# Performance work log

Measured on AMD Instinct MI355X. Metric: run time of the kernel, lower is better.

The kernel has to match this reference:

```python
import jax, jax.numpy as jnp
import numpy as np

NA, NW, H = 20000, 100000, 128
DA, DW = 64, 128
E_CR, E_IN, E_CO = 400000, 600000, 300000


def _seg_softmax(logits, seg, n):
    m = jax.ops.segment_max(logits, seg, num_segments=n)
    e = jnp.exp(logits - m[seg])
    s = jax.ops.segment_sum(e, seg, num_segments=n)
    return e / (s[seg] + 1e-16)


def _gat(x_src, x_dst, edge, W, b, a_s, a_d):
    # PyG GATConv, heads=1, concat=False, shared lin for src/dst, add_self_loops=True
    n_src, n_dst = x_src.shape[0], x_dst.shape[0]
    loops = jnp.arange(min(n_src, n_dst), dtype=edge.dtype)
    src = jnp.concatenate([edge[0], loops])
    dst = jnp.concatenate([edge[1], loops])
    hs = x_src @ W            # [n_src, H]
    hd = x_dst @ W            # [n_dst, H]
    logit = jax.nn.leaky_relu((hs @ a_s)[src] + (hd @ a_d)[dst], 0.2)
    alpha = _seg_softmax(logit, dst, n_dst)          # softmax over in-neighborhoods
    out = jax.ops.segment_sum(alpha[:, None] * hs[src], dst, num_segments=n_dst)
    return out + b


def _mlp2(x, w1, b1, w2, b2):
    return jax.nn.relu(x @ w1 + b1) @ w2 + b2


def setup_inputs() -> dict:
    key = jax.random.key(0)
    ks = iter(jax.random.split(key, 40))

    def p(shape, scale=0.1):
        return jax.random.normal(next(ks), shape, jnp.float32) * scale

    def edges(n_src, n_dst, E):
        s = jax.random.randint(next(ks), (E,), 0, n_src, dtype=jnp.int32)
        d = jax.random.randint(next(ks), (E,), 0, n_dst, dtype=jnp.int32)
        d = jnp.where(s == d, (d + 1) % n_dst, d)  # keep input loop-free (PyG strips them)
        return jnp.stack([s, d])

    e_creates = edges(NA, NW, E_CR)
    inp = {
        'artist_feat': jax.random.normal(next(ks), (NA, DA), jnp.float32),
        'work_feat': jax.random.normal(next(ks), (NW, DW), jnp.float32),
        'a_w1': p((DA, H)), 'a_b1': jnp.zeros(H, jnp.float32),
        'a_w2': p((H, H)), 'a_b2': jnp.zeros(H, jnp.float32),
        'w_w1': p((DW, H)), 'w_b1': jnp.zeros(H, jnp.float32),
        'w_w2': p((H, H)), 'w_b2': jnp.zeros(H, jnp.float32),
        'cr_W': p((H, H)), 'cr_b': jnp.zeros(H, jnp.float32), 'cr_as': p((H,)), 'cr_ad': p((H,)),
        'in_W': p((H, H)), 'in_b': jnp.zeros(H, jnp.float32), 'in_as': p((H,)), 'in_ad': p((H,)),
        'co_W': p((H, H)), 'co_b': jnp.zeros(H, jnp.float32), 'co_as': p((H,)), 'co_ad': p((H,)),
        'p_w1': p((2 * H, 256)), 'p_b1': jnp.zeros(256, jnp.float32),
        'p_w2': p((256, 128)), 'p_b2': jnp.zeros(128, jnp.float32),
        'p_w3': p((128, 1)), 'p_b3': jnp.zeros(1, jnp.float32),
        'e_creates': e_creates,
        'e_created_by': jnp.flip(e_creates, axis=0),  # reverse relation [work, artist]
        'e_infl': edges(NW, NW, E_IN),
        'e_collab': edges(NA, NA, E_CO),
    }
    return inp


def reference(artist_feat, work_feat,
              a_w1, a_b1, a_w2, a_b2,
              w_w1, w_b1, w_w2, w_b2,
              cr_W, cr_b, cr_as, cr_ad,
              in_W, in_b, in_as, in_ad,
              co_W, co_b, co_as, co_ad,
              p_w1, p_b1, p_w2, p_b2, p_w3, p_b3,
              e_creates, e_created_by, e_infl, e_collab):
    ax = _mlp2(artist_feat, a_w1, a_b1, a_w2, a_b2)      # [NA, H]
    wx = _mlp2(work_feat, w_w1, w_b1, w_w2, w_b2)        # [NW, H]
    wx = jax.nn.elu(_gat(ax, wx, e_creates, cr_W, cr_b, cr_as, cr_ad))
    wx = jax.nn.elu(_gat(wx, wx, e_infl, in_W, in_b, in_as, in_ad))
    au = _gat(wx, ax, e_created_by, cr_W, cr_b, cr_as, cr_ad)  # no elu (matches source)
    ac = jax.nn.elu(_gat(au, au, e_collab, co_W, co_b, co_as, co_ad))
    comb = jnp.concatenate([au, ac], axis=1)             # [NA, 2H]
    h = jax.nn.relu(comb @ p_w1 + p_b1)                  # dropout is identity in eval
    h = jax.nn.relu(h @ p_w2 + p_b2)
    return (h @ p_w3 + p_b3).squeeze()
```

## Files before the change

### kernel.cpp

```cpp
#include <hip/hip_runtime.h>
#include <hip/hip_bf16.h>
#include <cstddef>

#define NA 20000
#define NW 100000
#define HH 128
#define DA 64
#define E_CR 400000
#define E_IN 600000
#define E_CO 300000

#define ROW1 0
#define ROW2 (NW)
#define ROW3 (2 * NW)
#define ROW4 (2 * NW + NA)
#define NTOT (2 * NW + 2 * NA)
#define CAPW 40
#define CAPA 88
#define NPREP (10 * 128 + 1)
#define GNB ((NA + 127) / 128)

typedef short v8s __attribute__((ext_vector_type(8)));
typedef float v4f __attribute__((ext_vector_type(4)));

constexpr int PSLOT = 2 * 128 * 264;

__device__ inline short f2bf(float x) {
    union { float f; unsigned u; } c; c.f = x;
    unsigned r = c.u + 0x7fff + ((c.u >> 16) & 1);
    return (short)(r >> 16);
}
__device__ inline float bf2f(short s) {
    union { unsigned u; float f; } c; c.u = ((unsigned)(unsigned short)s) << 16;
    return c.f;
}
__device__ inline float bfu2f(unsigned short s) {
    union { unsigned u; float f; } c; c.u = ((unsigned)s) << 16;
    return c.f;
}

__device__ inline void split8(const float* xv, v8s& h, v8s& l) {
#pragma unroll
    for (int p = 0; p < 4; ++p) {
        float2 xf; xf.x = xv[2 * p]; xf.y = xv[2 * p + 1];
        __hip_bfloat162 hb = __float22bfloat162_rn(xf);
        float2 hf = __bfloat1622float2(hb);
        float2 lf; lf.x = xf.x - hf.x; lf.y = xf.y - hf.y;
        __hip_bfloat162 lb = __float22bfloat162_rn(lf);
        union { __hip_bfloat162 b; short2 s; } uh, ul;
        uh.b = hb; ul.b = lb;
        h[2 * p] = uh.s.x; h[2 * p + 1] = uh.s.y;
        l[2 * p] = ul.s.x; l[2 * p + 1] = ul.s.y;
    }
}

struct AppChunk { const int* e; int E; int* pad; int cap; int* deg; };

__device__ inline void do_append(const AppChunk& ap, int bid) {
    int b0 = bid * 1024 + threadIdx.x;
    int s[4], d[4]; bool ok[4];
#pragma unroll
    for (int u = 0; u < 4; ++u) {
        int i = b0 + u * 256;
        ok[u] = i < ap.E;
        s[u] = 0; d[u] = 0;
        if (ok[u]) { s[u] = ap.e[i]; d[u] = ap.e[ap.E + i]; }
    }
    int p[4];
#pragma unroll
    for (int u = 0; u < 4; ++u) if (ok[u]) p[u] = atomicAdd(&ap.deg[d[u]], 1);
#pragma unroll
    for (int u = 0; u < 4; ++u)
        if (ok[u] && p[u] < ap.cap)
            ap.pad[(size_t)d[u] * ap.cap + p[u]] = s[u];
}

struct PrepDesc { const float* src; int ldw; int K; };
struct PrepArgs {
    PrepDesc d[10]; const float* wvW; const float* wvA; float* vd;
    const float* gX; const float* gB; float* gY; int gM;
};

__global__ __launch_bounds__(256) void k_prep_append(PrepArgs a, short* __restrict__ out,
                                                    AppChunk ap)
{
    __shared__ short Bs2[2 * 128 * 72];
    if (blockIdx.x >= NPREP + GNB) { do_append(ap, blockIdx.x - NPREP - GNB); return; }
    if (blockIdx.x >= NPREP) {
        int bid = blockIdx.x - NPREP;
        const int tid = threadIdx.x;
        const int wave = tid >> 6, lane = tid & 63;
        const int l15 = lane & 15, quad = lane >> 4;
        const int wrow = bid * 128 + wave * 32;
        for (int e = tid; e < 64 * 128; e += 256) {
            int n = e & 127, k = e >> 7;
            float x = a.d[0].src[(size_t)k * 128 + n];
            short h = f2bf(x);
            short l = f2bf(x - bf2f(h));
            Bs2[n * 72 + k] = h;
            Bs2[128 * 72 + n * 72 + k] = l;
        }
        v8s ah[2][2], al[2][2];
#pragma unroll
        for (int rf = 0; rf < 2; ++rf) {
            int r = wrow + rf * 16 + l15; if (r >= a.gM) r = a.gM - 1;
            const float* xp = a.gX + (size_t)r * DA + quad * 8;
#pragma unroll
            for (int kf = 0; kf < 2; ++kf) {
                float xv[8];
                *(float4*)&xv[0] = *(const float4*)(xp + kf * 32);
                *(float4*)&xv[4] = *(const float4*)(xp + kf * 32 + 4);
                split8(xv, ah[rf][kf], al[rf][kf]);
            }
        }
        __syncthreads();
        v4f acc[2][8];
#pragma unroll
        for (int rf = 0; rf < 2; ++rf)
#pragma unroll
            for (int cf = 0; cf < 8; ++cf) acc[rf][cf] = (v4f){0.f, 0.f, 0.f, 0.f};
#pragma unroll
        for (int kf = 0; kf < 2; ++kf) {
#pragma unroll
            for (int cf = 0; cf < 8; ++cf) {
                int coff = (cf * 16 + l15) * 72 + kf * 32 + quad * 8;
                v8s bh = *(const v8s*)&Bs2[coff];
                v8s bl = *(const v8s*)&Bs2[128 * 72 + coff];
#pragma unroll
                for (int rf = 0; rf < 2; ++rf) {
                    acc[rf][cf] = __builtin_amdgcn_mfma_f32_16x16x32_bf16(al[rf][kf], bh, acc[rf][cf], 0, 0, 0);
                    acc[rf][cf] = __builtin_amdgcn_mfma_f32_16x16x32_bf16(ah[rf][kf], bl, acc[rf][cf], 0, 0, 0);
                    acc[rf][cf] = __builtin_amdgcn_mfma_f32_16x16x32_bf16(ah[rf][kf], bh, acc[rf][cf], 0, 0, 0);
                }
            }
        }
        float bv[8];
#pragma unroll
        for (int cf = 0; cf < 8; ++cf) bv[cf] = a.gB[cf * 16 + l15];
#pragma unroll
        for (int rf = 0; rf < 2; ++rf) {
#pragma unroll
            for (int reg = 0; reg < 4; ++reg) {
                int r = wrow + rf * 16 + quad * 4 + reg;
                if (r >= a.gM) continue;
                float* yp = a.gY + (size_t)r * HH;
#pragma unroll
                for (int cf = 0; cf < 8; ++cf) {
                    float o = acc[rf][cf][reg] + bv[cf];
                    yp[cf * 16 + l15] = o > 0.f ? o : 0.f;
                }
            }
        }
        return;
    }
    if (blockIdx.x == NPREP - 1) {
        __shared__ float sa[HH];
        int t = threadIdx.x;
        if (t < HH) sa[t] = a.wvA[t];
        __syncthreads();
        if (t < HH) {
            float s = 0.f;
            for (int jj = 0; jj < HH; ++jj) s += a.wvW[(size_t)t * HH + jj] * sa[jj];
            a.vd[t] = s;
        }
        return;
    }
    int m = blockIdx.x >> 7;
    int e = (blockIdx.x & 127) * 256 + threadIdx.x;
    PrepDesc dd = a.d[m];
    int K = dd.K;
    int KP = (K <= 128) ? K + 8 : K;
    if (e >= K * 128) return;
    int n = e & 127, k = e >> 7;
    float x = dd.src[(size_t)k * dd.ldw + n];
    short h = f2bf(x);
    short l = f2bf(x - bf2f(h));
    short* base = out + (size_t)m * PSLOT;
    base[n * KP + k] = h;
    base[128 * KP + n * KP + k] = l;
}

template<int K, int ACT, int NSS, int ST, int LDSB, int OBF, int DUAL>
__global__ __launch_bounds__(256, 2) void k_mfma(
    const float* __restrict__ X, int ldx,
    const short* __restrict__ Wp,
    const float* __restrict__ bias,
    float* __restrict__ Y, int ldy, int M,
    const float* __restrict__ v1, float* __restrict__ ss1,
    const float* __restrict__ v2, float* __restrict__ ss2,
    const float* __restrict__ sb)
{
    constexpr int KF = K / 32;
    constexpr int KP = LDSB ? K + 8 : K;
    __shared__ short Bs[LDSB ? 2 * 128 * (K + 8) : 8];
    const int tid = threadIdx.x;
    const int wave = tid >> 6, lane = tid & 63;
    const int l15 = lane & 15, quad = lane >> 4;
    int bid = blockIdx.x;
    if (DUAL) {
        int g0 = gridDim.x >> 1;
        if (bid >= g0) { bid -= g0; Wp += PSLOT; bias += 128; Y += 128; }
    }
    const int wrow = bid * 128 + wave * 32;

    if (LDSB) {
        const float4* src = (const float4*)Wp;
        float4* dst = (float4*)Bs;
        constexpr int total = 2 * 128 * KP / 8;
        for (int i = tid; i < total; i += 256) dst[i] = src[i];
    }

    v4f acc[2][8];
#pragma unroll
    for (int rf = 0; rf < 2; ++rf)
#pragma unroll
        for (int cf = 0; cf < 8; ++cf) acc[rf][cf] = (v4f){0.f, 0.f, 0.f, 0.f};

    if (LDSB) {
        v8s ah[2][KF], al[2][KF];
#pragma unroll
        for (int rf = 0; rf < 2; ++rf) {
            int r = wrow + rf * 16 + l15; if (r >= M) r = M - 1;
            const float* xp = X + (size_t)r * ldx + quad * 8;
#pragma unroll
            for (int kf = 0; kf < KF; ++kf) {
                float xv[8];
                *(float4*)&xv[0] = *(const float4*)(xp + kf * 32);
                *(float4*)&xv[4] = *(const float4*)(xp + kf * 32 + 4);
                split8(xv, ah[rf][kf], al[rf][kf]);
            }
        }
        __syncthreads();
#pragma unroll
        for (int kf = 0; kf < KF; ++kf) {
#pragma unroll
            for (int cf = 0; cf < 8; ++cf) {
                const short* bp = &Bs[(cf * 16 + l15) * KP + kf * 32 + quad * 8];
                v8s bh = *(const v8s*)bp;
                v8s bl = *(const v8s*)(bp + 128 * KP);
#pragma unroll
                for (int rf = 0; rf < 2; ++rf) {
                    acc[rf][cf] = __builtin_amdgcn_mfma_f32_16x16x32_bf16(al[rf][kf], bh, acc[rf][cf], 0, 0, 0);
                    acc[rf][cf] = __builtin_amdgcn_mfma_f32_16x16x32_bf16(ah[rf][kf], bl, acc[rf][cf], 0, 0, 0);
                    acc[rf][cf] = __builtin_amdgcn_mfma_f32_16x16x32_bf16(ah[rf][kf], bh, acc[rf][cf], 0, 0, 0);
                }
            }
        }
    } else {
        for (int kf = 0; kf < KF; ++kf) {
            v8s ah[2], al[2];
#pragma unroll
            for (int rf = 0; rf < 2; ++rf) {
                int r = wrow + rf * 16 + l15; if (r >= M) r = M - 1;
                const float* xp = X + (size_t)r * ldx + kf * 32 + quad * 8;
                float xv[8];
                *(float4*)&xv[0] = *(const float4*)xp;
                *(float4*)&xv[4] = *(const float4*)(xp + 4);
                split8(xv, ah[rf], al[rf]);
            }
#pragma unroll
            for (int cf = 0; cf < 8; ++cf) {
                const short* bp = Wp + (size_t)(cf * 16 + l15) * K + kf * 32 + quad * 8;
                v8s bh = *(const v8s*)bp;
                v8s bl = *(const v8s*)(bp + 128 * KP);
#pragma unroll
                for (int rf = 0; rf < 2; ++rf) {
                    acc[rf][cf] = __builtin_amdgcn_mfma_f32_16x16x32_bf16(al[rf], bh, acc[rf][cf], 0, 0, 0);
                    acc[rf][cf] = __builtin_amdgcn_mfma_f32_16x16x32_bf16(ah[rf], bl, acc[rf][cf], 0, 0, 0);
                    acc[rf][cf] = __builtin_amdgcn_mfma_f32_16x16x32_bf16(ah[rf], bh, acc[rf][cf], 0, 0, 0);
                }
            }
        }
    }

    float bv[8], v1c[8], v2c[8];
#pragma unroll
    for (int cf = 0; cf < 8; ++cf) {
        int col = cf * 16 + l15;
        bv[cf] = bias ? bias[col] : 0.f;
        if (NSS >= 1) v1c[cf] = v1[col];
        if (NSS >= 2) v2c[cf] = v2[col];
    }
    float sbv = (NSS >= 1 && sb) ? sb[0] : 0.f;

#pragma unroll
    for (int rf = 0; rf < 2; ++rf) {
#pragma unroll
        for (int reg = 0; reg < 4; ++reg) {
            int r = wrow + rf * 16 + quad * 4 + reg;
            if (r >= M) continue;
            float p1 = 0.f, p2 = 0.f;
#pragma unroll
            for (int cf = 0; cf < 8; ++cf) {
                float o = acc[rf][cf][reg] + bv[cf];
                if (ACT == 1) o = o > 0.f ? o : 0.f;
                if (NSS >= 1) p1 = fmaf(o, v1c[cf], p1);
                if (NSS >= 2) p2 = fmaf(o, v2c[cf], p2);
                if (ST) {
                    if (OBF) ((unsigned short*)Y)[(size_t)r * ldy + cf * 16 + l15] = (unsigned short)f2bf(o);
                    else     Y[(size_t)r * ldy + cf * 16 + l15] = o;
                }
            }
            if (NSS >= 1) {
#pragma unroll
                for (int w = 1; w < 16; w <<= 1) {
                    p1 += __shfl_xor(p1, w, 64);
                    if (NSS >= 2) p2 += __shfl_xor(p2, w, 64);
                }
                if (l15 == 0) {
                    ss1[r] = p1 + sbv;
                    if (NSS >= 2) ss2[r] = p2;
                }
            }
        }
    }
}

struct MfmaCfg {
    const float* X; int ldx;
    const short* Wp;
    const float* bias;
    float* Y; int ldy; int M;
    int act, nss, obf;
    const float* v1; float* ss1;
    const float* v2; float* ss2;
    int nblocks;
};

__global__ __launch_bounds__(256, 2) void k_mfma2(MfmaCfg c0, MfmaCfg c1, AppChunk ap)
{
    constexpr int KF = 4, KP = 136;
    __shared__ short Bs[2 * 128 * KP];
    int bid = blockIdx.x;
    if (bid >= c0.nblocks + c1.nblocks) { do_append(ap, bid - c0.nblocks - c1.nblocks); return; }
    const bool first = bid < c0.nblocks;
    const MfmaCfg& c = first ? c0 : c1;
    if (!first) bid -= c0.nblocks;
    const int tid = threadIdx.x;
    const int wave = tid >> 6, lane = tid & 63;
    const int l15 = lane & 15, quad = lane >> 4;
    const int wrow = bid * 128 + wave * 32;

    {
        const float4* src = (const float4*)c.Wp;
        float4* dst = (float4*)Bs;
        constexpr int total = 2 * 128 * KP / 8;
        for (int i = tid; i < total; i += 256) dst[i] = src[i];
    }

    v4f acc[2][8];
#pragma unroll
    for (int rf = 0; rf < 2; ++rf)
#pragma unroll
        for (int cf = 0; cf < 8; ++cf) acc[rf][cf] = (v4f){0.f, 0.f, 0.f, 0.f};

    v8s ah[2][KF], al[2][KF];
#pragma unroll
    for (int rf = 0; rf < 2; ++rf) {
        int r = wrow + rf * 16 + l15; if (r >= c.M) r = c.M - 1;
        const float* xp = c.X + (size_t)r * c.ldx + quad * 8;
#pragma unroll
        for (int kf = 0; kf < KF; ++kf) {
            float xv[8];
            *(float4*)&xv[0] = *(const float4*)(xp + kf * 32);
            *(float4*)&xv[4] = *(const float4*)(xp + kf * 32 + 4);
            split8(xv, ah[rf][kf], al[rf][kf]);
        }
    }
    __syncthreads();
#pragma unroll
    for (int kf = 0; kf < KF; ++kf) {
#pragma unroll
        for (int cf = 0; cf < 8; ++cf) {
            const short* bp = &Bs[(cf * 16 + l15) * KP + kf * 32 + quad * 8];
            v8s bh = *(const v8s*)bp;
            v8s bl = *(const v8s*)(bp + 128 * KP);
#pragma unroll
            for (int rf = 0; rf < 2; ++rf) {
                acc[rf][cf] = __builtin_amdgcn_mfma_f32_16x16x32_bf16(al[rf][kf], bh, acc[rf][cf], 0, 0, 0);
                acc[rf][cf] = __builtin_amdgcn_mfma_f32_16x16x32_bf16(ah[rf][kf], bl, acc[rf][cf], 0, 0, 0);
                acc[rf][cf] = __builtin_amdgcn_mfma_f32_16x16x32_bf16(ah[rf][kf], bh, acc[rf][cf], 0, 0, 0);
            }
        }
    }

    float bv[8], v1c[8], v2c[8];
#pragma unroll
    for (int cf = 0; cf < 8; ++cf) {
        int col = cf * 16 + l15;
        bv[cf] = c.bias ? c.bias[col] : 0.f;
        v1c[cf] = (c.nss >= 1) ? c.v1[col] : 0.f;
        v2c[cf] = (c.nss >= 2) ? c.v2[col] : 0.f;
    }

#pragma unroll
    for (int rf = 0; rf < 2; ++rf) {
#pragma unroll
        for (int reg = 0; reg < 4; ++reg) {
            int r = wrow + rf * 16 + quad * 4 + reg;
            if (r >= c.M) continue;
            float p1 = 0.f, p2 = 0.f;
#pragma unroll
            for (int cf = 0; cf < 8; ++cf) {
                float o = acc[rf][cf][reg] + bv[cf];
                if (c.act) o = o > 0.f ? o : 0.f;
                p1 = fmaf(o, v1c[cf], p1);
                p2 = fmaf(o, v2c[cf], p2);
                if (c.obf) ((unsigned short*)c.Y)[(size_t)r * c.ldy + cf * 16 + l15] = (unsigned short)f2bf(o);
                else       c.Y[(size_t)r * c.ldy + cf * 16 + l15] = o;
            }
            if (c.nss >= 1) {
#pragma unroll
                for (int w = 1; w < 16; w <<= 1) {
                    p1 += __shfl_xor(p1, w, 64);
                    p2 += __shfl_xor(p2, w, 64);
                }
                if (l15 == 0) {
                    c.ss1[r] = p1;
                    if (c.nss >= 2) c.ss2[r] = p2;
                }
            }
        }
    }
}

template<int ELU, int U, int CAP>
__global__ __launch_bounds__(256) void k_aggregate(
    const int* __restrict__ deg, const int* __restrict__ esp,
    const unsigned short* __restrict__ hs, const float* __restrict__ ss,
    const float* __restrict__ sd, const float* __restrict__ bias,
    float* __restrict__ out, int ldy, int n, int loopn)
{
    int lane = threadIdx.x & 63;
    int wv = threadIdx.x >> 6;
    int d = blockIdx.x * 4 + wv;
    if (d >= n) return;
    int half = lane >> 5;
    int col = (lane & 31) * 4;
    const int* row = esp + (size_t)d * CAP;
    int i1 = deg[d]; if (i1 > CAP) i1 = CAP;
    float sdv = sd[d];
    float den = 0.f;
    float ax = 0.f, ay = 0.f, az = 0.f, aw = 0.f;
    if (half == 0 && d < loopn) {
        ushort4 h = *(const ushort4*)(hs + (size_t)d * HH + col);
        float l = ss[d] + sdv;
        l = l < 0.f ? 0.2f * l : l;
        float e = __expf(l);
        den += e;
        ax = fmaf(e, bfu2f(h.x), ax);
        ay = fmaf(e, bfu2f(h.y), ay);
        az = fmaf(e, bfu2f(h.z), az);
        aw = fmaf(e, bfu2f(h.w), aw);
    }
    int i = 0;
    for (; i + 2 * U <= i1; i += 2 * U) {
        int s[U]; ushort4 h[U]; float sv[U];
#pragma unroll
        for (int u = 0; u < U; ++u) s[u] = row[i + 2 * u + half];
#pragma unroll
        for (int u = 0; u < U; ++u) h[u] = *(const ushort4*)(hs + (size_t)s[u] * HH + col);
#pragma unroll
        for (int u = 0; u < U; ++u) sv[u] = ss[s[u]];
#pragma unroll
        for (int u = 0; u < U; ++u) {
            float l = sv[u] + sdv;
            l = l < 0.f ? 0.2f * l : l;
            float e = __expf(l);
            den += e;
            ax = fmaf(e, bfu2f(h[u].x), ax);
            ay = fmaf(e, bfu2f(h[u].y), ay);
            az = fmaf(e, bfu2f(h[u].z), az);
            aw = fmaf(e, bfu2f(h[u].w), aw);
        }
    }
    if (i < i1) {
        int s[U]; ushort4 h[U]; float sv[U]; bool act[U];
#pragma unroll
        for (int u = 0; u < U; ++u) {
            int idx = i + 2 * u + half;
            act[u] = idx < i1;
            s[u] = row[act[u] ? idx : (i1 - 1)];
        }
#pragma unroll
        for (int u = 0; u < U; ++u) h[u] = *(const ushort4*)(hs + (size_t)s[u] * HH + col);
#pragma unroll
        for (int u = 0; u < U; ++u) sv[u] = ss[s[u]];
#pragma unroll
        for (int u = 0; u < U; ++u) {
            float l = sv[u] + sdv;
            l = l < 0.f ? 0.2f * l : l;
            float e = act[u] ? __expf(l) : 0.f;
            den += e;
            ax = fmaf(e, bfu2f(h[u].x), ax);
            ay = fmaf(e, bfu2f(h[u].y), ay);
            az = fmaf(e, bfu2f(h[u].z), az);
            aw = fmaf(e, bfu2f(h[u].w), aw);
        }
    }
    den += __shfl_xor(den, 32, 64);
    ax += __shfl_xor(ax, 32, 64);
    ay += __shfl_xor(ay, 32, 64);
    az += __shfl_xor(az, 32, 64);
    aw += __shfl_xor(aw, 32, 64);
    if (half == 0) {
        float4 b = *(const float4*)(bias + col);
        float inv = 1.f / (den + 1e-16f);
        float o0 = ax * inv + b.x;
        float o1 = ay * inv + b.y;
        float o2 = az * inv + b.z;
        float o3 = aw * inv + b.w;
        if (ELU) {
            o0 = o0 > 0.f ? o0 : expm1f(o0);
            o1 = o1 > 0.f ? o1 : expm1f(o1);
            o2 = o2 > 0.f ? o2 : expm1f(o2);
            o3 = o3 > 0.f ? o3 : expm1f(o3);
        }
        *(float4*)(out + (size_t)d * ldy + col) = make_float4(o0, o1, o2, o3);
    }
}

extern "C" void kernel_launch(void* const* d_in, const int* in_sizes, int n_in,
                              void* d_out, int out_size, void* d_ws, size_t ws_size,
                              hipStream_t stream)
{
    const float* artist = (const float*)d_in[0];
    const float* workf  = (const float*)d_in[1];
    const float* a_w1 = (const float*)d_in[2];  const float* a_b1 = (const float*)d_in[3];
    const float* a_w2 = (const float*)d_in[4];  const float* a_b2 = (const float*)d_in[5];
    const float* w_w1 = (const float*)d_in[6];  const float* w_b1 = (const float*)d_in[7];
    const float* w_w2 = (const float*)d_in[8];  const float* w_b2 = (const float*)d_in[9];
    const float* cr_W = (const float*)d_in[10]; const float* cr_b = (const float*)d_in[11];
    const float* cr_as = (const float*)d_in[12]; const float* cr_ad = (const float*)d_in[13];
    const float* in_W = (const float*)d_in[14]; const float* in_b = (const float*)d_in[15];
    const float* in_as = (const float*)d_in[16]; const float* in_ad = (const float*)d_in[17];
    const float* co_W = (const float*)d_in[18]; const float* co_b = (const float*)d_in[19];
    const float* co_as = (const float*)d_in[20]; const float* co_ad = (const float*)d_in[21];
    const float* p_w1 = (const float*)d_in[22]; const float* p_b1 = (const float*)d_in[23];
    const float* p_w2 = (const float*)d_in[24]; const float* p_b2 = (const float*)d_in[25];
    const float* p_w3 = (const float*)d_in[26]; const float* p_b3 = (const float*)d_in[27];
    const int* e_cr = (const int*)d_in[28];
    const int* e_cb = (const int*)d_in[29];
    const int* e_in = (const int*)d_in[30];
    const int* e_co = (const int*)d_in[31];

    char* wsp = (char*)d_ws;
    size_t off = 0;
    auto alloc = [&](size_t bytes) -> void* {
        void* p = wsp + off;
        off += (bytes + 255) / 256 * 256;
        return p;
    };
    float* ax   = (float*)alloc((size_t)NA * HH * 4);
    float* hsA  = (float*)alloc((size_t)NA * HH * 4);
    float* wx   = (float*)alloc((size_t)NW * HH * 4);
    float* hs   = (float*)alloc((size_t)NW * HH * 4);
    unsigned short* hsb = (unsigned short*)alloc((size_t)NW * HH * 2);
    float* comb = (float*)alloc((size_t)NA * 256 * 4);
    float* ss1 = (float*)alloc((size_t)NA * 4);
    float* sd1 = (float*)alloc((size_t)NW * 4);
    float* ss2 = (float*)alloc((size_t)NW * 4);
    float* sd2 = (float*)alloc((size_t)NW * 4);
    float* ss3 = (float*)alloc((size_t)NW * 4);
    float* sd3 = (float*)alloc((size_t)NA * 4);
    float* ss4 = (float*)alloc((size_t)NA * 4);
    float* sd4 = (float*)alloc((size_t)NA * 4);
    float* vd  = (float*)alloc(HH * 4);
    int* deg   = (int*)alloc((size_t)NTOT * 4);
    int* pad1  = (int*)alloc((size_t)NW * CAPW * 4);
    int* pad2  = (int*)alloc((size_t)NW * CAPW * 4);
    int* pad3  = (int*)alloc((size_t)NA * CAPA * 4);
    int* pad4  = (int*)alloc((size_t)NA * CAPA * 4);
    short* preW = (short*)alloc((size_t)10 * PSLOT * 2);
    (void)ws_size; (void)in_sizes; (void)n_in; (void)out_size;

    auto pre = [&](int m) { return preW + (size_t)m * PSLOT; };
    auto gg = [](int M) { return (M + 127) / 128; };
    auto apb = [](int E) { return (E + 1023) / 1024; };
    const float* nf = nullptr;
    float* nfm = nullptr;

    PrepArgs pa;
    pa.d[0] = {a_w1, HH, DA};
    pa.d[1] = {a_w2, HH, HH};
    pa.d[2] = {w_w1, HH, HH};
    pa.d[3] = {w_w2, HH, HH};
    pa.d[4] = {cr_W, HH, HH};
    pa.d[5] = {in_W, HH, HH};
    pa.d[6] = {co_W, HH, HH};
    pa.d[7] = {p_w1, 256, 256};
    pa.d[8] = {p_w1 + 128, 256, 256};
    pa.d[9] = {p_w2, HH, 256};
    pa.wvW = cr_W; pa.wvA = cr_ad; pa.vd = vd;
    pa.gX = artist; pa.gB = a_b1; pa.gY = hsA; pa.gM = NA;

    AppChunk ap1 = {e_cr, E_CR, pad1, CAPW, deg + ROW1};
    AppChunk ap2 = {e_in, E_IN, pad2, CAPW, deg + ROW2};
    AppChunk ap3 = {e_cb, E_CR, pad3, CAPA, deg + ROW3};
    AppChunk ap4 = {e_co, E_CO, pad4, CAPA, deg + ROW4};

    (void)hipMemsetAsync(deg, 0, (size_t)NTOT * 4, stream);

    k_prep_append<<<NPREP + GNB + apb(E_CR), 256, 0, stream>>>(pa, preW, ap1);

    {
        MfmaCfg c0 = {workf, HH, pre(2), w_b1, hs, HH, NW, 1, 0, 0, nf, nfm, nf, nfm, gg(NW)};
        MfmaCfg c1 = {hsA, HH, pre(1), a_b2, ax, HH, NA, 0, 1, 0, vd, sd3, nf, nfm, gg(NA)};
        k_mfma2<<<gg(NW) + gg(NA) + apb(E_IN), 256, 0, stream>>>(c0, c1, ap2);
    }
    {
        MfmaCfg c0 = {hs, HH, pre(3), w_b2, wx, HH, NW, 0, 1, 0, vd, sd1, nf, nfm, gg(NW)};
        MfmaCfg c1 = {ax, HH, pre(4), nullptr, (float*)hsb, HH, NA, 0, 1, 1, cr_as, ss1, nf, nfm, gg(NA)};
        k_mfma2<<<gg(NW) + gg(NA) + apb(E_CR), 256, 0, stream>>>(c0, c1, ap3);
    }

    k_aggregate<1, 2, CAPW><<<(NW + 3) / 4, 256, 0, stream>>>(deg + ROW1, pad1, hsb, ss1, sd1, cr_b, wx, HH, NW, NA);

    {
        MfmaCfg c0 = {wx, HH, pre(5), nullptr, (float*)hsb, HH, NW, 0, 2, 1, in_as, ss2, in_ad, sd2, gg(NW)};
        MfmaCfg c1 = {nullptr, 0, nullptr, nullptr, nullptr, 0, 0, 0, 0, 0, nf, nfm, nf, nfm, 0};
        k_mfma2<<<gg(NW) + apb(E_CO), 256, 0, stream>>>(c0, c1, ap4);
    }
    k_aggregate<1, 2, CAPW><<<(NW + 3) / 4, 256, 0, stream>>>(deg + ROW2, pad2, hsb, ss2, sd2, in_b, wx, HH, NW, NW);

    k_mfma<HH, 0, 1, 1, 1, 1, 0><<<gg(NW), 256, 0, stream>>>(wx, HH, pre(4), nullptr, (float*)hsb, HH, NW, cr_as, ss3, nf, nfm, nf);
    k_aggregate<0, 4, CAPA><<<(NA + 3) / 4, 256, 0, stream>>>(deg + ROW3, pad3, hsb, ss3, sd3, cr_b, comb, 256, NA, NA);

    k_mfma<HH, 0, 2, 1, 1, 1, 0><<<gg(NA), 256, 0, stream>>>(comb, 256, pre(6), nullptr, (float*)hsb, HH, NA, co_as, ss4, co_ad, sd4, nf);
    k_aggregate<1, 4, CAPA><<<(NA + 3) / 4, 256, 0, stream>>>(deg + ROW4, pad4, hsb, ss4, sd4, co_b, comb + 128, 256, NA, NA);

    float* h1 = hs;
    k_mfma<256, 1, 0, 1, 0, 0, 1><<<2 * gg(NA), 256, 0, stream>>>(comb, 256, pre(7), p_b1, h1, 256, NA, nf, nfm, nf, nfm, nf);
    k_mfma<256, 1, 1, 0, 0, 0, 0><<<gg(NA), 256, 0, stream>>>(h1, 256, pre(9), p_b2, nfm, 0, NA, p_w3, (float*)d_out, nf, nfm, p_b3);
}
```

Baseline: 590.3 us.

## Store work-node intermediates in bf16 and skip the low-part MFMA for bf16 inputs

The work-node MLP hidden layer (hsw) and the GAT outputs for work nodes (wxb) are now stored as bf16 instead of fp32. Matmuls that read them load bf16 directly and drop the al*bh term of the split-precision three-MFMA scheme. The second work MLP layer no longer stores wx, since only its attention scalar is used downstream, and a dedicated h1 buffer is allocated. This roughly halves HBM traffic for the large NW×128 tensors and cuts MFMA work, in exchange for bf16 rounding of intermediate activations, which may loosen accuracy.

```diff
diff --git a/kernel.cpp b/kernel.cpp
--- a/kernel.cpp
+++ b/kernel.cpp
@@ -180,7 +180,7 @@
     base[128 * KP + n * KP + k] = l;
 }
 
-template<int K, int ACT, int NSS, int ST, int LDSB, int OBF, int DUAL>
+template<int K, int ACT, int NSS, int ST, int LDSB, int OBF, int DUAL, int XBF>
 __global__ __launch_bounds__(256, 2) void k_mfma(
     const float* __restrict__ X, int ldx,
     const short* __restrict__ Wp,
@@ -216,11 +216,16 @@
 #pragma unroll
         for (int cf = 0; cf < 8; ++cf) acc[rf][cf] = (v4f){0.f, 0.f, 0.f, 0.f};
 
-    if (LDSB) {
-        v8s ah[2][KF], al[2][KF];
-#pragma unroll
-        for (int rf = 0; rf < 2; ++rf) {
-            int r = wrow + rf * 16 + l15; if (r >= M) r = M - 1;
+    v8s ah[2][KF], al[2][KF];
+#pragma unroll
+    for (int rf = 0; rf < 2; ++rf) {
+        int r = wrow + rf * 16 + l15; if (r >= M) r = M - 1;
+        if (XBF) {
+            const unsigned short* xp = (const unsigned short*)X + (size_t)r * ldx + quad * 8;
+#pragma unroll
+            for (int kf = 0; kf < KF; ++kf)
+                ah[rf][kf] = *(const v8s*)(xp + kf * 32);
+        } else {
             const float* xp = X + (size_t)r * ldx + quad * 8;
 #pragma unroll
             for (int kf = 0; kf < KF; ++kf) {
@@ -230,45 +235,21 @@
                 split8(xv, ah[rf][kf], al[rf][kf]);
             }
         }
-        __syncthreads();
-#pragma unroll
-        for (int kf = 0; kf < KF; ++kf) {
-#pragma unroll
-            for (int cf = 0; cf < 8; ++cf) {
-                const short* bp = &Bs[(cf * 16 + l15) * KP + kf * 32 + quad * 8];
-                v8s bh = *(const v8s*)bp;
-                v8s bl = *(const v8s*)(bp + 128 * KP);
-#pragma unroll
-                for (int rf = 0; rf < 2; ++rf) {
-                    acc[rf][cf] = __builtin_amdgcn_mfma_f32_16x16x32_bf16(al[rf][kf], bh, acc[rf][cf], 0, 0, 0);
-                    acc[rf][cf] = __builtin_amdgcn_mfma_f32_16x16x32_bf16(ah[rf][kf], bl, acc[rf][cf], 0, 0, 0);
-                    acc[rf][cf] = __builtin_amdgcn_mfma_f32_16x16x32_bf16(ah[rf][kf], bh, acc[rf][cf], 0, 0, 0);
-                }
-            }
-        }
-    } else {
-        for (int kf = 0; kf < KF; ++kf) {
-            v8s ah[2], al[2];
+    }
+    if (LDSB) __syncthreads();
+#pragma unroll
+    for (int kf = 0; kf < KF; ++kf) {
+#pragma unroll
+        for (int cf = 0; cf < 8; ++cf) {
+            const short* bp = LDSB ? &Bs[(cf * 16 + l15) * KP + kf * 32 + quad * 8]
+                                   : Wp + (size_t)(cf * 16 + l15) * K + kf * 32 + quad * 8;
+            v8s bh = *(const v8s*)bp;
+            v8s bl = *(const v8s*)(bp + 128 * KP);
 #pragma unroll
             for (int rf = 0; rf < 2; ++rf) {
-                int r = wrow + rf * 16 + l15; if (r >= M) r = M - 1;
-                const float* xp = X + (size_t)r * ldx + kf * 32 + quad * 8;
-                float xv[8];
-                *(float4*)&xv[0] = *(const float4*)xp;
-                *(float4*)&xv[4] = *(const float4*)(xp + 4);
-                split8(xv, ah[rf], al[rf]);
-            }
-#pragma unroll
-            for (int cf = 0; cf < 8; ++cf) {
-                const short* bp = Wp + (size_t)(cf * 16 + l15) * K + kf * 32 + quad * 8;
-                v8s bh = *(const v8s*)bp;
-                v8s bl = *(const v8s*)(bp + 128 * KP);
-#pragma unroll
-                for (int rf = 0; rf < 2; ++rf) {
-                    acc[rf][cf] = __builtin_amdgcn_mfma_f32_16x16x32_bf16(al[rf], bh, acc[rf][cf], 0, 0, 0);
-                    acc[rf][cf] = __builtin_amdgcn_mfma_f32_16x16x32_bf16(ah[rf], bl, acc[rf][cf], 0, 0, 0);
-                    acc[rf][cf] = __builtin_amdgcn_mfma_f32_16x16x32_bf16(ah[rf], bh, acc[rf][cf], 0, 0, 0);
-                }
+                if (!XBF) acc[rf][cf] = __builtin_amdgcn_mfma_f32_16x16x32_bf16(al[rf][kf], bh, acc[rf][cf], 0, 0, 0);
+                acc[rf][cf] = __builtin_amdgcn_mfma_f32_16x16x32_bf16(ah[rf][kf], bl, acc[rf][cf], 0, 0, 0);
+                acc[rf][cf] = __builtin_amdgcn_mfma_f32_16x16x32_bf16(ah[rf][kf], bh, acc[rf][cf], 0, 0, 0);
             }
         }
     }
@@ -321,7 +302,7 @@
     const short* Wp;
     const float* bias;
     float* Y; int ldy; int M;
-    int act, nss, obf;
+    int act, nss, obf, xbf, st;
     const float* v1; float* ss1;
     const float* v2; float* ss2;
     int nblocks;
@@ -358,13 +339,22 @@
 #pragma unroll
     for (int rf = 0; rf < 2; ++rf) {
         int r = wrow + rf * 16 + l15; if (r >= c.M) r = c.M - 1;
-        const float* xp = c.X + (size_t)r * c.ldx + quad * 8;
-#pragma unroll
-        for (int kf = 0; kf < KF; ++kf) {
-            float xv[8];
-            *(float4*)&xv[0] = *(const float4*)(xp + kf * 32);
-            *(float4*)&xv[4] = *(const float4*)(xp + kf * 32 + 4);
-            split8(xv, ah[rf][kf], al[rf][kf]);
+        if (c.xbf) {
+            const unsigned short* xp = (const unsigned short*)c.X + (size_t)r * c.ldx + quad * 8;
+#pragma unroll
+            for (int kf = 0; kf < KF; ++kf) {
+                ah[rf][kf] = *(const v8s*)(xp + kf * 32);
+                al[rf][kf] = (v8s)(short)0;
+            }
+        } else {
+            const float* xp = c.X + (size_t)r * c.ldx + quad * 8;
+#pragma unroll
+            for (int kf = 0; kf < KF; ++kf) {
+                float xv[8];
+                *(float4*)&xv[0] = *(const float4*)(xp + kf * 32);
+                *(float4*)&xv[4] = *(const float4*)(xp + kf * 32 + 4);
+                split8(xv, ah[rf][kf], al[rf][kf]);
+            }
         }
     }
     __syncthreads();
@@ -377,7 +367,7 @@
             v8s bl = *(const v8s*)(bp + 128 * KP);
 #pragma unroll
             for (int rf = 0; rf < 2; ++rf) {
-                acc[rf][cf] = __builtin_amdgcn_mfma_f32_16x16x32_bf16(al[rf][kf], bh, acc[rf][cf], 0, 0, 0);
+                if (!c.xbf) acc[rf][cf] = __builtin_amdgcn_mfma_f32_16x16x32_bf16(al[rf][kf], bh, acc[rf][cf], 0, 0, 0);
                 acc[rf][cf] = __builtin_amdgcn_mfma_f32_16x16x32_bf16(ah[rf][kf], bl, acc[rf][cf], 0, 0, 0);
                 acc[rf][cf] = __builtin_amdgcn_mfma_f32_16x16x32_bf16(ah[rf][kf], bh, acc[rf][cf], 0, 0, 0);
             }
@@ -406,8 +396,10 @@
                 if (c.act) o = o > 0.f ? o : 0.f;
                 p1 = fmaf(o, v1c[cf], p1);
                 p2 = fmaf(o, v2c[cf], p2);
-                if (c.obf) ((unsigned short*)c.Y)[(size_t)r * c.ldy + cf * 16 + l15] = (unsigned short)f2bf(o);
-                else       c.Y[(size_t)r * c.ldy + cf * 16 + l15] = o;
+                if (c.st) {
+                    if (c.obf) ((unsigned short*)c.Y)[(size_t)r * c.ldy + cf * 16 + l15] = (unsigned short)f2bf(o);
+                    else       c.Y[(size_t)r * c.ldy + cf * 16 + l15] = o;
+                }
             }
             if (c.nss >= 1) {
 #pragma unroll
@@ -424,12 +416,12 @@
     }
 }
 
-template<int ELU, int U, int CAP>
+template<int ELU, int U, int CAP, int OBF>
 __global__ __launch_bounds__(256) void k_aggregate(
     const int* __restrict__ deg, const int* __restrict__ esp,
     const unsigned short* __restrict__ hs, const float* __restrict__ ss,
     const float* __restrict__ sd, const float* __restrict__ bias,
-    float* __restrict__ out, int ldy, int n, int loopn)
+    void* __restrict__ out, int ldy, int n, int loopn)
 {
     int lane = threadIdx.x & 63;
     int wv = threadIdx.x >> 6;
@@ -516,7 +508,16 @@
             o2 = o2 > 0.f ? o2 : expm1f(o2);
             o3 = o3 > 0.f ? o3 : expm1f(o3);
         }
-        *(float4*)(out + (size_t)d * ldy + col) = make_float4(o0, o1, o2, o3);
+        if (OBF) {
+            ushort4 ob;
+            ob.x = (unsigned short)f2bf(o0);
+            ob.y = (unsigned short)f2bf(o1);
+            ob.z = (unsigned short)f2bf(o2);
+            ob.w = (unsigned short)f2bf(o3);
+            *(ushort4*)((unsigned short*)out + (size_t)d * ldy + col) = ob;
+        } else {
+            *(float4*)((float*)out + (size_t)d * ldy + col) = make_float4(o0, o1, o2, o3);
+        }
     }
 }
 
@@ -553,9 +554,10 @@
     };
     float* ax   = (float*)alloc((size_t)NA * HH * 4);
     float* hsA  = (float*)alloc((size_t)NA * HH * 4);
-    float* wx   = (float*)alloc((size_t)NW * HH * 4);
-    float* hs   = (float*)alloc((size_t)NW * HH * 4);
+    unsigned short* hsw = (unsigned short*)alloc((size_t)NW * HH * 2);
+    unsigned short* wxb = (unsigned short*)alloc((size_t)NW * HH * 2);
     unsigned short* hsb = (unsigned short*)alloc((size_t)NW * HH * 2);
+    float* h1   = (float*)alloc((size_t)NA * 256 * 4);
     float* comb = (float*)alloc((size_t)NA * 256 * 4);
     float* ss1 = (float*)alloc((size_t)NA * 4);
     float* sd1 = (float*)alloc((size_t)NW * 4);
@@ -604,32 +606,31 @@
     k_prep_append<<<NPREP + GNB + apb(E_CR), 256, 0, stream>>>(pa, preW, ap1);
 
     {
-        MfmaCfg c0 = {workf, HH, pre(2), w_b1, hs, HH, NW, 1, 0, 0, nf, nfm, nf, nfm, gg(NW)};
-        MfmaCfg c1 = {hsA, HH, pre(1), a_b2, ax, HH, NA, 0, 1, 0, vd, sd3, nf, nfm, gg(NA)};
+        MfmaCfg c0 = {workf, HH, pre(2), w_b1, (float*)hsw, HH, NW, 1, 0, 1, 0, 1, nf, nfm, nf, nfm, gg(NW)};
+        MfmaCfg c1 = {hsA, HH, pre(1), a_b2, ax, HH, NA, 0, 1, 0, 0, 1, vd, sd3, nf, nfm, gg(NA)};
         k_mfma2<<<gg(NW) + gg(NA) + apb(E_IN), 256, 0, stream>>>(c0, c1, ap2);
     }
     {
-        MfmaCfg c0 = {hs, HH, pre(3), w_b2, wx, HH, NW, 0, 1, 0, vd, sd1, nf, nfm, gg(NW)};
-        MfmaCfg c1 = {ax, HH, pre(4), nullptr, (float*)hsb, HH, NA, 0, 1, 1, cr_as, ss1, nf, nfm, gg(NA)};
+        MfmaCfg c0 = {(const float*)hsw, HH, pre(3), w_b2, nfm, HH, NW, 0, 1, 0, 1, 0, vd, sd1, nf, nfm, gg(NW)};
+        MfmaCfg c1 = {ax, HH, pre(4), nullptr, (float*)hsb, HH, NA, 0, 1, 1, 0, 1, cr_as, ss1, nf, nfm, gg(NA)};
         k_mfma2<<<gg(NW) + gg(NA) + apb(E_CR), 256, 0, stream>>>(c0, c1, ap3);
     }
 
-    k_aggregate<1, 2, CAPW><<<(NW + 3) / 4, 256, 0, stream>>>(deg + ROW1, pad1, hsb, ss1, sd1, cr_b, wx, HH, NW, NA);
+    k_aggregate<1, 2, CAPW, 1><<<(NW + 3) / 4, 256, 0, stream>>>(deg + ROW1, pad1, hsb, ss1, sd1, cr_b, wxb, HH, NW, NA);
 
     {
-        MfmaCfg c0 = {wx, HH, pre(5), nullptr, (float*)hsb, HH, NW, 0, 2, 1, in_as, ss2, in_ad, sd2, gg(NW)};
-        MfmaCfg c1 = {nullptr, 0, nullptr, nullptr, nullptr, 0, 0, 0, 0, 0, nf, nfm, nf, nfm, 0};
+        MfmaCfg c0 = {(const float*)wxb, HH, pre(5), nullptr, (float*)hsb, HH, NW, 0, 2, 1, 1, 1, in_as, ss2, in_ad, sd2, gg(NW)};
+        MfmaCfg c1 = {nullptr, 0, nullptr, nullptr, nullptr, 0, 0, 0, 0, 0, 0, 0, nf, nfm, nf, nfm, 0};
         k_mfma2<<<gg(NW) + apb(E_CO), 256, 0, stream>>>(c0, c1, ap4);
     }
-    k_aggregate<1, 2, CAPW><<<(NW + 3) / 4, 256, 0, stream>>>(deg + ROW2, pad2, hsb, ss2, sd2, in_b, wx, HH, NW, NW);
-
-    k_mfma<HH, 0, 1, 1, 1, 1, 0><<<gg(NW), 256, 0, stream>>>(wx, HH, pre(4), nullptr, (float*)hsb, HH, NW, cr_as, ss3, nf, nfm, nf);
-    k_aggregate<0, 4, CAPA><<<(NA + 3) / 4, 256, 0, stream>>>(deg + ROW3, pad3, hsb, ss3, sd3, cr_b, comb, 256, NA, NA);
-
-    k_mfma<HH, 0, 2, 1, 1, 1, 0><<<gg(NA), 256, 0, stream>>>(comb, 256, pre(6), nullptr, (float*)hsb, HH, NA, co_as, ss4, co_ad, sd4, nf);
-    k_aggregate<1, 4, CAPA><<<(NA + 3) / 4, 256, 0, stream>>>(deg + ROW4, pad4, hsb, ss4, sd4, co_b, comb + 128, 256, NA, NA);
-
-    float* h1 = hs;
-    k_mfma<256, 1, 0, 1, 0, 0, 1><<<2 * gg(NA), 256, 0, stream>>>(comb, 256, pre(7), p_b1, h1, 256, NA, nf, nfm, nf, nfm, nf);
-    k_mfma<256, 1, 1, 0, 0, 0, 0><<<gg(NA), 256, 0, stream>>>(h1, 256, pre(9), p_b2, nfm, 0, NA, p_w3, (float*)d_out, nf, nfm, p_b3);
-}
+    k_aggregate<1, 2, CAPW, 1><<<(NW + 3) / 4, 256, 0, stream>>>(deg + ROW2, pad2, hsb, ss2, sd2, in_b, wxb, HH, NW, NW);
+
+    k_mfma<HH, 0, 1, 1, 1, 1, 0, 1><<<gg(NW), 256, 0, stream>>>((const float*)wxb, HH, pre(4), nullptr, (float*)hsb, HH, NW, cr_as, ss3, nf, nfm, nf);
+    k_aggregate<0, 4, CAPA, 0><<<(NA + 3) / 4, 256, 0, stream>>>(deg + ROW3, pad3, hsb, ss3, sd3, cr_b, comb, 256, NA, NA);
+
+    k_mfma<HH, 0, 2, 1, 1, 1, 0, 0><<<gg(NA), 256, 0, stream>>>(comb, 256, pre(6), nullptr, (float*)hsb, HH, NA, co_as, ss4, co_ad, sd4, nf);
+    k_aggregate<1, 4, CAPA, 0><<<(NA + 3) / 4, 256, 0, stream>>>(deg + ROW4, pad4, hsb, ss4, sd4, co_b, comb + 128, 256, NA, NA);
+
+    k_mfma<256, 1, 0, 1, 0, 0, 1, 0><<<2 * gg(NA), 256, 0, stream>>>(comb, 256, pre(7), p_b1, h1, 256, NA, nf, nfm, nf, nfm, nf);
+    k_mfma<256, 1, 1, 0, 0, 0, 0, 0><<<gg(NA), 256, 0, stream>>>(h1, 256, pre(9), p_b2, nfm, 0, NA, p_w3, (float*)d_out, nf, nfm, p_b3);
+}
```

Result: faster. 576.8 us (-2.3%).
